# Kernel tuning notes

Hardware: AMD Instinct MI355X
Metric: run time of the kernel (lower is better)

## Reference

```python
import jax, jax.numpy as jnp
import numpy as np

HID = 256

def _linear(x, W, b):
    # torch nn.Linear: x @ W.T + b
    return x @ W.T + b

def setup_inputs() -> dict:
    key = jax.random.key(0)
    ks = jax.random.split(key, 9)
    N = 8192
    s = 1.0 / np.sqrt(HID)
    inp = {
        'query': jax.random.normal(ks[0], (N, HID), dtype=jnp.float32),
        'key':   jax.random.normal(ks[1], (N, HID), dtype=jnp.float32),
        'value': jax.random.normal(ks[2], (N, HID), dtype=jnp.float32),
        'Wq': jax.random.uniform(ks[3], (HID, HID), jnp.float32, -s, s),
        'bq': jax.random.uniform(ks[4], (HID,), jnp.float32, -s, s),
        'Wk': jax.random.uniform(ks[5], (HID, HID), jnp.float32, -s, s),
        'bk': jax.random.uniform(ks[6], (HID,), jnp.float32, -s, s),
        'Wv': jax.random.uniform(ks[7], (HID, HID), jnp.float32, -s, s),
        'bv': jax.random.uniform(ks[8], (HID,), jnp.float32, -s, s),
    }
    return inp

def reference(query, key, value, Wq, bq, Wk, bk, Wv, bv):
    q = _linear(query, Wq, bq)            # [N, H]
    k = _linear(key, Wk, bk)              # [N, H]
    v = _linear(value, Wv, bv)            # [N, H]
    q = q.reshape(-1, HID)
    k = k.reshape(-1, HID)
    v = v.reshape(-1, HID)
    attn = jax.nn.sigmoid(q @ k.T)        # [N, N], sigmoid attention (no softmax)
    return attn @ v                       # [N, H]
```

## Files before the change

kernel.cpp:

```cpp
#include <hip/hip_runtime.h>
#include <hip/hip_bf16.h>
#include <stdint.h>

#define HID 256
#define NTOK 8192
#define NS 8
#define SLICE (NTOK / NS)
#define CHUNK 32
#define NCH (SLICE / CHUNK)

typedef unsigned short u16;
typedef unsigned int u32;
typedef __bf16 bf16x8 __attribute__((ext_vector_type(8)));
typedef float f32x16 __attribute__((ext_vector_type(16)));
typedef __fp16 h16x2 __attribute__((ext_vector_type(2)));

#define TAU(r, h) (((r) & 3) + 8 * ((r) >> 2) + 4 * (h))

__device__ __forceinline__ u16 f2bf(float f) {
  u32 u = __float_as_uint(f);
  return (u16)((u + 0x7FFFu + ((u >> 16) & 1u)) >> 16);
}

__device__ __forceinline__ u32 cvtpk_bf16(float a, float b) {
  u32 r;
  asm("v_cvt_pk_bf16_f32 %0, %1, %2" : "=v"(r) : "v"(a), "v"(b));
  return r;
}

__device__ __forceinline__ u32 cvtpk_f16(float a, float b) {
  union { h16x2 h; u32 u; } cv;
  cv.h = __builtin_amdgcn_cvt_pkrtz(a, b);
  return cv.u;
}

__global__ void wcvt_kernel(const float* __restrict__ Wq, const float* __restrict__ Wk,
                            const float* __restrict__ Wv, u16* __restrict__ out) {
  int idx = blockIdx.x * 256 + threadIdx.x;
  int mat = idx >> 14;
  int off = (idx & 16383) << 2;
  const float* src = mat == 0 ? Wq : (mat == 1 ? Wk : Wv);
  float4 v = *reinterpret_cast<const float4*>(src + off);
  ushort4 o;
  o.x = f2bf(v.x); o.y = f2bf(v.y); o.z = f2bf(v.z); o.w = f2bf(v.w);
  *reinterpret_cast<ushort4*>(out + mat * 65536 + off) = o;
}

__global__ __launch_bounds__(256, 2) void proj_kernel(
    const float* __restrict__ Xq, const float* __restrict__ Xk, const float* __restrict__ Xv,
    const u16* __restrict__ wcvt,
    const float* __restrict__ Bq, const float* __restrict__ Bk, const float* __restrict__ Bv,
    u16* __restrict__ oq, u16* __restrict__ ok, u16* __restrict__ ovt)
{
  __shared__ __attribute__((aligned(16))) unsigned char smem[32768 + 4 * 4352];
  u16* wbuf0 = (u16*)smem;
  u16* wbuf1 = (u16*)(smem + 16384);
  float* scratch = (float*)(smem + 32768 + (threadIdx.x >> 6) * 4352);

  const int tid = threadIdx.x, bid = blockIdx.x;
  const int sel = bid >> 7;
  const int m0 = (bid & 127) << 6;
  const int wid = tid >> 6, l = tid & 63;
  const int l31 = l & 31, lh = l >> 5;
  const int wrow = wid & 1;
  const int wcol = wid >> 1;

  const float* X = sel == 0 ? Xq : (sel == 1 ? Xk : Xv);
  const u16* W = wcvt + sel * 65536;
  const float* B = sel == 0 ? Bq : (sel == 1 ? Bk : Bv);
  const int mrow = m0 + wrow * 32 + l31;

  f32x16 acc[4];
#pragma unroll
  for (int nt = 0; nt < 4; ++nt) acc[nt] = (f32x16)0.f;

  auto stageW = [&](int kc, u16* buf) {
#pragma unroll
    for (int ii = 0; ii < 4; ++ii) {
      int u = (wid * 4 + ii) * 64 + l;
      int ol = u >> 8, n = u & 255;
      const u16* g = W + n * HID + kc * 32 + ol * 8;
      __builtin_amdgcn_global_load_lds((const __attribute__((address_space(1))) u32*)g,
                                       (__attribute__((address_space(3))) u32*)(buf + (size_t)u * 8),
                                       16, 0, 0);
    }
  };

  stageW(0, wbuf0);
  __syncthreads();
  for (int kc = 0; kc < 8; ++kc) {
    u16* cur = (kc & 1) ? wbuf1 : wbuf0;
    if (kc < 7) stageW(kc + 1, (kc & 1) ? wbuf0 : wbuf1);
#pragma unroll
    for (int k2 = 0; k2 < 2; ++k2) {
      int ks = kc * 2 + k2;
      float4 a0 = *reinterpret_cast<const float4*>(X + (size_t)mrow * HID + ks * 16 + lh * 8);
      float4 a1 = *reinterpret_cast<const float4*>(X + (size_t)mrow * HID + ks * 16 + lh * 8 + 4);
      union { u16 u[8]; bf16x8 v; } au;
      au.u[0] = f2bf(a0.x); au.u[1] = f2bf(a0.y); au.u[2] = f2bf(a0.z); au.u[3] = f2bf(a0.w);
      au.u[4] = f2bf(a1.x); au.u[5] = f2bf(a1.y); au.u[6] = f2bf(a1.z); au.u[7] = f2bf(a1.w);
#pragma unroll
      for (int nt = 0; nt < 4; ++nt) {
        int unit = (k2 * 2 + lh) * 256 + (wcol * 4 + nt) * 32 + l31;
        bf16x8 b = *reinterpret_cast<bf16x8*>(cur + (size_t)unit * 8);
        acc[nt] = __builtin_amdgcn_mfma_f32_32x32x16_bf16(au.v, b, acc[nt], 0, 0, 0);
      }
    }
    __syncthreads();
  }

#pragma unroll
  for (int nt = 0; nt < 4; ++nt) {
    const int colblk = wcol * 4 + nt;
    float bv = B[colblk * 32 + l31];
#pragma unroll
    for (int r = 0; r < 16; ++r)
      scratch[TAU(r, lh) * 33 + l31] = acc[nt][r] + bv;
    if (sel < 2) {
      u16* o = sel == 0 ? oq : ok;
      u16 tmp[16];
#pragma unroll
      for (int c = 0; c < 16; ++c) tmp[c] = f2bf(scratch[l31 * 33 + lh * 16 + c]);
      u16* dst = o + (size_t)mrow * HID + colblk * 32 + lh * 16;
      *reinterpret_cast<uint4*>(dst) = *reinterpret_cast<uint4*>(&tmp[0]);
      *reinterpret_cast<uint4*>(dst + 8) = *reinterpret_cast<uint4*>(&tmp[8]);
    } else {
      u16 tmp[16];
#pragma unroll
      for (int c = 0; c < 16; ++c) tmp[c] = f2bf(scratch[(lh * 16 + c) * 33 + l31]);
      u16* dst = ovt + (size_t)(colblk * 32 + l31) * NTOK + m0 + wrow * 32 + lh * 16;
      *reinterpret_cast<uint4*>(dst) = *reinterpret_cast<uint4*>(&tmp[0]);
      *reinterpret_cast<uint4*>(dst + 8) = *reinterpret_cast<uint4*>(&tmp[8]);
    }
  }
}

__global__ __launch_bounds__(256, 2) void attn_kernel(
    const u16* __restrict__ qw, const u16* __restrict__ kw,
    const u16* __restrict__ vtw, u16* __restrict__ partial)
{
  __shared__ __attribute__((aligned(16))) unsigned char smem[65536];
  u16* kb0 = (u16*)smem;            u16* kb1 = (u16*)(smem + 16384);
  u16* vb0 = (u16*)(smem + 32768);  u16* vb1 = (u16*)(smem + 49152);

  const int tid = threadIdx.x, bid = blockIdx.x;
  const int slice = bid & 7, qt = bid >> 3;
  const int q0 = qt * 128;
  const int tokbase = slice * SLICE;
  const int wq = tid >> 6, l = tid & 63;
  const int l31 = l & 31, lh = l >> 5;
  const int qrow = q0 + wq * 32 + l31;

  bf16x8 qB[16];
#pragma unroll
  for (int ks = 0; ks < 16; ++ks)
    qB[ks] = *reinterpret_cast<const bf16x8*>(qw + (size_t)qrow * HID + ks * 16 + lh * 8);

  auto stageK = [&](int c, u16* buf) {
    int tok0 = tokbase + c * CHUNK;
#pragma unroll
    for (int ii = 0; ii < 4; ++ii) {
      int u = (wq * 4 + ii) * 64 + l;
      int o = u >> 5, t = u & 31;
      const u16* g = kw + (size_t)(tok0 + t) * HID + o * 8;
      __builtin_amdgcn_global_load_lds((const __attribute__((address_space(1))) u32*)g,
                                       (__attribute__((address_space(3))) u32*)(buf + (size_t)u * 8),
                                       16, 0, 0);
    }
  };
  auto stageV = [&](int c, u16* buf) {
    int tok0 = tokbase + c * CHUNK;
#pragma unroll
    for (int ii = 0; ii < 4; ++ii) {
      int u = (wq * 4 + ii) * 64 + l;
      int j = u >> 8, d = u & 255;
      const u16* g = vtw + (size_t)d * NTOK + tok0 + j * 8;
      __builtin_amdgcn_global_load_lds((const __attribute__((address_space(1))) u32*)g,
                                       (__attribute__((address_space(3))) u32*)(buf + (size_t)u * 8),
                                       16, 0, 0);
    }
  };

  f32x16 oacc[8];
#pragma unroll
  for (int dt = 0; dt < 8; ++dt) oacc[dt] = (f32x16)0.f;

  stageK(0, kb0);
  stageV(0, vb0);
  __syncthreads();

  for (int c = 0; c < NCH; ++c) {
    u16* kc_ = (c & 1) ? kb1 : kb0;
    u16* vc_ = (c & 1) ? vb1 : vb0;
    if (c + 1 < NCH) {
      stageK(c + 1, (c & 1) ? kb0 : kb1);
      stageV(c + 1, (c & 1) ? vb0 : vb1);
    }

    f32x16 sacc = (f32x16)0.f;
#pragma unroll
    for (int ks = 0; ks < 16; ++ks) {
      bf16x8 kf = *reinterpret_cast<bf16x8*>(kc_ + (size_t)((ks * 2 + lh) * 32 + l31) * 8);
      sacc = __builtin_amdgcn_mfma_f32_32x32x16_bf16(kf, qB[ks], sacc, 0, 0, 0);
    }

    float p[16];
#pragma unroll
    for (int r = 0; r < 16; ++r) {
      float e = __expf(-sacc[r]);
      p[r] = __builtin_amdgcn_rcpf(1.0f + e);
    }

    u32 w0[4], w1[4];
    {
      u32 x0 = cvtpk_bf16(p[0], p[1]),  y0 = cvtpk_bf16(p[4], p[5]);
      asm volatile("v_permlane32_swap_b32 %0, %1" : "+v"(x0), "+v"(y0));
      u32 x1 = cvtpk_bf16(p[2], p[3]),  y1 = cvtpk_bf16(p[6], p[7]);
      asm volatile("v_permlane32_swap_b32 %0, %1" : "+v"(x1), "+v"(y1));
      w0[0] = x0; w0[1] = x1; w0[2] = y0; w0[3] = y1;
      u32 x2 = cvtpk_bf16(p[8], p[9]),  y2 = cvtpk_bf16(p[12], p[13]);
      asm volatile("v_permlane32_swap_b32 %0, %1" : "+v"(x2), "+v"(y2));
      u32 x3 = cvtpk_bf16(p[10], p[11]), y3 = cvtpk_bf16(p[14], p[15]);
      asm volatile("v_permlane32_swap_b32 %0, %1" : "+v"(x3), "+v"(y3));
      w1[0] = x2; w1[1] = x3; w1[2] = y2; w1[3] = y3;
    }

#pragma unroll
    for (int kp = 0; kp < 2; ++kp) {
      union { u32 u[4]; bf16x8 v; } pb;
      pb.u[0] = kp ? w1[0] : w0[0]; pb.u[1] = kp ? w1[1] : w0[1];
      pb.u[2] = kp ? w1[2] : w0[2]; pb.u[3] = kp ? w1[3] : w0[3];
#pragma unroll
      for (int dt = 0; dt < 8; ++dt) {
        bf16x8 vf = *reinterpret_cast<bf16x8*>(vc_ + (size_t)((kp * 2 + lh) * 256 + dt * 32 + l31) * 8);
        oacc[dt] = __builtin_amdgcn_mfma_f32_32x32x16_bf16(vf, pb.v, oacc[dt], 0, 0, 0);
      }
    }

    __syncthreads();
  }

  float* scratch = (float*)(smem + wq * 4352);
  u16* part = partial + (size_t)slice * NTOK * HID;
#pragma unroll
  for (int dt = 0; dt < 8; ++dt) {
#pragma unroll
    for (int r = 0; r < 16; ++r)
      scratch[TAU(r, lh) * 33 + l31] = oacc[dt][r];
    u32 pk[8];
#pragma unroll
    for (int c2 = 0; c2 < 8; ++c2) {
      float f0 = scratch[(lh * 16 + 2 * c2) * 33 + l31];
      float f1 = scratch[(lh * 16 + 2 * c2 + 1) * 33 + l31];
      pk[c2] = cvtpk_f16(f0, f1);
    }
    u16* dst = part + (size_t)qrow * HID + dt * 32 + lh * 16;
    *reinterpret_cast<uint4*>(dst) = *reinterpret_cast<uint4*>(&pk[0]);
    *reinterpret_cast<uint4*>(dst + 8) = *reinterpret_cast<uint4*>(&pk[4]);
  }
}

__global__ void reduce_kernel(const u16* __restrict__ partial, float* __restrict__ out) {
  size_t idx = (size_t)blockIdx.x * 256 + threadIdx.x;
  size_t base = idx * 8;
  float a[8] = {0.f, 0.f, 0.f, 0.f, 0.f, 0.f, 0.f, 0.f};
#pragma unroll
  for (int s = 0; s < NS; ++s) {
    uint4 v = *reinterpret_cast<const uint4*>(partial + (size_t)s * NTOK * HID + base);
    const __fp16* h = (const __fp16*)&v;
#pragma unroll
    for (int e = 0; e < 8; ++e) a[e] += (float)h[e];
  }
  *reinterpret_cast<float4*>(out + base) = make_float4(a[0], a[1], a[2], a[3]);
  *reinterpret_cast<float4*>(out + base + 4) = make_float4(a[4], a[5], a[6], a[7]);
}

extern "C" void kernel_launch(void* const* d_in, const int* in_sizes, int n_in,
                              void* d_out, int out_size, void* d_ws, size_t ws_size,
                              hipStream_t stream) {
  const float* query = (const float*)d_in[0];
  const float* key_  = (const float*)d_in[1];
  const float* value = (const float*)d_in[2];
  const float* Wq = (const float*)d_in[3];
  const float* bq = (const float*)d_in[4];
  const float* Wk = (const float*)d_in[5];
  const float* bk = (const float*)d_in[6];
  const float* Wv = (const float*)d_in[7];
  const float* bv = (const float*)d_in[8];
  float* out = (float*)d_out;

  unsigned char* ws = (unsigned char*)d_ws;
  u16* qws  = (u16*)(ws);
  u16* kws  = (u16*)(ws + (4u << 20));
  u16* vtws = (u16*)(ws + (8u << 20));
  u16* wcvt = (u16*)(ws + (12u << 20));
  u16* part = (u16*)(ws + (13u << 20));

  wcvt_kernel<<<192, 256, 0, stream>>>(Wq, Wk, Wv, wcvt);
  proj_kernel<<<384, 256, 0, stream>>>(query, key_, value, wcvt, bq, bk, bv,
                                       qws, kws, vtws);
  attn_kernel<<<512, 256, 0, stream>>>(qws, kws, vtws, part);
  reduce_kernel<<<1024, 256, 0, stream>>>(part, out);
}
```

Before: 195.5 us.

## Stage X tiles through LDS in projection and split QK accumulator chain in attention

In the projection kernel, input rows are now prefetched into double-buffered, XOR-swizzled LDS with async global-to-LDS loads, and converted with packed bf16 conversion instead of per-lane direct global loads. The occupancy hint is raised from 2 to 3 blocks per CU. In the attention kernel, the 16-step QK MFMA chain is split across four independent accumulators that are summed afterwards, which breaks the serial dependency. The MFMA sections are also wrapped in s_setprio to favour issue. The extra LDS use and registers may limit the occupancy the new launch bound asks for, and the split sums add a few VALU adds per chunk.

```diff
diff --git a/kernel.cpp b/kernel.cpp
--- a/kernel.cpp
+++ b/kernel.cpp
@@ -46,7 +46,7 @@
   *reinterpret_cast<ushort4*>(out + mat * 65536 + off) = o;
 }
 
-__global__ __launch_bounds__(256, 2) void proj_kernel(
+__global__ __launch_bounds__(256, 3) void proj_kernel(
     const float* __restrict__ Xq, const float* __restrict__ Xk, const float* __restrict__ Xv,
     const u16* __restrict__ wcvt,
     const float* __restrict__ Bq, const float* __restrict__ Bk, const float* __restrict__ Bv,
@@ -68,7 +68,9 @@
   const float* X = sel == 0 ? Xq : (sel == 1 ? Xk : Xv);
   const u16* W = wcvt + sel * 65536;
   const float* B = sel == 0 ? Bq : (sel == 1 ? Bk : Bv);
-  const int mrow = m0 + wrow * 32 + l31;
+  const int rloc = wrow * 32 + l31;
+
+  auto Xs = [&](int b) -> float* { return (float*)(smem + 32768 + b * 8192); };
 
   f32x16 acc[4];
 #pragma unroll
@@ -85,20 +87,36 @@
                                        16, 0, 0);
     }
   };
+  auto stageX = [&](int kc, float* buf) {
+#pragma unroll
+    for (int ii = 0; ii < 2; ++ii) {
+      int u = (wid * 2 + ii) * 64 + l;
+      int row = u >> 3, seg = u & 7;
+      const float* g = X + (size_t)(m0 + row) * HID + kc * 32 + ((seg ^ (row & 7)) << 2);
+      __builtin_amdgcn_global_load_lds((const __attribute__((address_space(1))) u32*)g,
+                                       (__attribute__((address_space(3))) u32*)(buf + (size_t)u * 4),
+                                       16, 0, 0);
+    }
+  };
 
   stageW(0, wbuf0);
+  stageX(0, Xs(0));
   __syncthreads();
   for (int kc = 0; kc < 8; ++kc) {
     u16* cur = (kc & 1) ? wbuf1 : wbuf0;
-    if (kc < 7) stageW(kc + 1, (kc & 1) ? wbuf0 : wbuf1);
+    float* xcur = Xs(kc & 1);
+    if (kc < 7) {
+      stageW(kc + 1, (kc & 1) ? wbuf0 : wbuf1);
+      stageX(kc + 1, Xs((kc & 1) ^ 1));
+    }
 #pragma unroll
     for (int k2 = 0; k2 < 2; ++k2) {
-      int ks = kc * 2 + k2;
-      float4 a0 = *reinterpret_cast<const float4*>(X + (size_t)mrow * HID + ks * 16 + lh * 8);
-      float4 a1 = *reinterpret_cast<const float4*>(X + (size_t)mrow * HID + ks * 16 + lh * 8 + 4);
-      union { u16 u[8]; bf16x8 v; } au;
-      au.u[0] = f2bf(a0.x); au.u[1] = f2bf(a0.y); au.u[2] = f2bf(a0.z); au.u[3] = f2bf(a0.w);
-      au.u[4] = f2bf(a1.x); au.u[5] = f2bf(a1.y); au.u[6] = f2bf(a1.z); au.u[7] = f2bf(a1.w);
+      int seg0 = k2 * 4 + lh * 2;
+      float4 xa = reinterpret_cast<const float4*>(xcur)[rloc * 8 + (seg0 ^ (rloc & 7))];
+      float4 xb = reinterpret_cast<const float4*>(xcur)[rloc * 8 + ((seg0 + 1) ^ (rloc & 7))];
+      union { u32 u[4]; bf16x8 v; } au;
+      au.u[0] = cvtpk_bf16(xa.x, xa.y); au.u[1] = cvtpk_bf16(xa.z, xa.w);
+      au.u[2] = cvtpk_bf16(xb.x, xb.y); au.u[3] = cvtpk_bf16(xb.z, xb.w);
 #pragma unroll
       for (int nt = 0; nt < 4; ++nt) {
         int unit = (k2 * 2 + lh) * 256 + (wcol * 4 + nt) * 32 + l31;
@@ -121,7 +139,7 @@
       u16 tmp[16];
 #pragma unroll
       for (int c = 0; c < 16; ++c) tmp[c] = f2bf(scratch[l31 * 33 + lh * 16 + c]);
-      u16* dst = o + (size_t)mrow * HID + colblk * 32 + lh * 16;
+      u16* dst = o + (size_t)(m0 + rloc) * HID + colblk * 32 + lh * 16;
       *reinterpret_cast<uint4*>(dst) = *reinterpret_cast<uint4*>(&tmp[0]);
       *reinterpret_cast<uint4*>(dst + 8) = *reinterpret_cast<uint4*>(&tmp[8]);
     } else {
@@ -197,12 +215,17 @@
       stageV(c + 1, (c & 1) ? vb0 : vb1);
     }
 
-    f32x16 sacc = (f32x16)0.f;
+    f32x16 sc4[4];
+#pragma unroll
+    for (int i = 0; i < 4; ++i) sc4[i] = (f32x16)0.f;
+    __builtin_amdgcn_s_setprio(1);
 #pragma unroll
     for (int ks = 0; ks < 16; ++ks) {
       bf16x8 kf = *reinterpret_cast<bf16x8*>(kc_ + (size_t)((ks * 2 + lh) * 32 + l31) * 8);
-      sacc = __builtin_amdgcn_mfma_f32_32x32x16_bf16(kf, qB[ks], sacc, 0, 0, 0);
-    }
+      sc4[ks & 3] = __builtin_amdgcn_mfma_f32_32x32x16_bf16(kf, qB[ks], sc4[ks & 3], 0, 0, 0);
+    }
+    __builtin_amdgcn_s_setprio(0);
+    f32x16 sacc = (sc4[0] + sc4[1]) + (sc4[2] + sc4[3]);
 
     float p[16];
 #pragma unroll
@@ -225,6 +248,7 @@
       w1[0] = x2; w1[1] = x3; w1[2] = y2; w1[3] = y3;
     }
 
+    __builtin_amdgcn_s_setprio(1);
 #pragma unroll
     for (int kp = 0; kp < 2; ++kp) {
       union { u32 u[4]; bf16x8 v; } pb;
@@ -236,6 +260,7 @@
         oacc[dt] = __builtin_amdgcn_mfma_f32_32x32x16_bf16(vf, pb.v, oacc[dt], 0, 0, 0);
       }
     }
+    __builtin_amdgcn_s_setprio(0);
 
     __syncthreads();
   }
```

After: 245.3 us. 25.5% more time.
